# Optimization experiments

Measured on AMD Instinct MI355X. Metric: run time of the kernel, lower is better.

## Reference

```python
import jax, jax.numpy as jnp
import numpy as np

KERNEL_MUL = 2.0
KERNEL_NUM = 5
EPS = 1e-06


def setup_inputs() -> dict:
    key = jax.random.key(0)
    k1, k2 = jax.random.split(key)
    N, D = 4096, 256
    source = jax.random.normal(k1, (N, D), dtype=jnp.float32)
    target = jax.random.normal(k2, (N, D), dtype=jnp.float32)
    return {"source": source, "target": target}


def reference(source, target):
    n_src = source.shape[0]
    total = jnp.concatenate([source, target], axis=0)  # [2N, D]
    n = total.shape[0]
    # the broadcasted (total0 - total1)**2 sum, without the O(N^2*D) tensor).
    sq = jnp.sum(total * total, axis=1)  # [2N]
    L2 = sq[:, None] + sq[None, :] - 2.0 * (total @ total.T)  # [2N, 2N]
    # Bandwidth from detached distances (torch uses L2_distance.data).
    bandwidth = jax.lax.stop_gradient(jnp.sum(L2)) / (n * n - n)
    bandwidth = bandwidth / (KERNEL_MUL ** (KERNEL_NUM // 2))
    kernels = jnp.zeros_like(L2)
    for i in range(KERNEL_NUM):
        bw = bandwidth * (KERNEL_MUL ** i)
        kernels = kernels + jnp.exp(-L2 / (bw + EPS))
    XX = kernels[:n_src, :n_src]
    YY = kernels[n_src:, n_src:]
    XY = kernels[:n_src, n_src:]
    YX = kernels[n_src:, :n_src]
    return jnp.mean(XX + YY - XY - YX)
```

## Files before the change

### kernel.cpp

```cpp
#include <hip/hip_runtime.h>

#define N_TOT 8192
#define NS 4096
#define D 256
#define NB 64
#define NTRI (NB*(NB+1)/2)
#define HALF_B 32

typedef float f32x16 __attribute__((ext_vector_type(16)));
typedef float f32x2 __attribute__((ext_vector_type(2)));
typedef int i32x4 __attribute__((ext_vector_type(4)));
typedef int i32x8 __attribute__((ext_vector_type(8)));

__device__ __forceinline__ void gload16(const void* g, void* l) {
  __builtin_amdgcn_global_load_lds(
      (const __attribute__((address_space(1))) unsigned int*)g,
      (__attribute__((address_space(3))) unsigned int*)l,
      16, 0, 0);
}

__global__ void k_prep(const float* __restrict__ src, const float* __restrict__ tgt,
                       unsigned char* __restrict__ Xb, float* __restrict__ sqv,
                       float* __restrict__ pm, float* __restrict__ wsqp) {
  __shared__ float colacc[256];
  __shared__ float wred[4];
  int t = threadIdx.x, l = t & 63, w = t >> 6;
  colacc[t] = 0.f;
  __syncthreads();
  int base = blockIdx.x * 32;
  float c0 = 0.f, c1 = 0.f, c2 = 0.f, c3 = 0.f;
  float wsq = 0.f;
  #pragma unroll
  for (int r = 0; r < 8; ++r) {
    int row = base + w * 8 + r;
    const float* p = (row < NS) ? (src + (size_t)row * D) : (tgt + (size_t)(row - NS) * D);
    float4 v = ((const float4*)p)[l];
    int pk = __builtin_amdgcn_cvt_pk_fp8_f32(v.x, v.y, 0, false);
    pk = __builtin_amdgcn_cvt_pk_fp8_f32(v.z, v.w, pk, true);
    ((int*)(Xb + (size_t)row * D))[l] = pk;
    c0 += v.x; c1 += v.y; c2 += v.z; c3 += v.w;
    float s = fmaf(v.x, v.x, fmaf(v.y, v.y, fmaf(v.z, v.z, v.w * v.w)));
    for (int o = 32; o > 0; o >>= 1) s += __shfl_down(s, o, 64);
    if (l == 0) { sqv[row] = s; wsq += s; }
  }
  atomicAdd(&colacc[4 * l + 0], c0);
  atomicAdd(&colacc[4 * l + 1], c1);
  atomicAdd(&colacc[4 * l + 2], c2);
  atomicAdd(&colacc[4 * l + 3], c3);
  if (l == 0) wred[w] = wsq;
  __syncthreads();
  pm[blockIdx.x * 256 + t] = colacc[t];
  if (t == 0) wsqp[blockIdx.x] = (wred[0] + wred[1]) + (wred[2] + wred[3]);
}

__global__ void k_bw(const float* __restrict__ pm, const float* __restrict__ wsqp,
                     float* __restrict__ coef) {
  __shared__ double red[256];
  int t = threadIdx.x;
  float cs = 0.f;
  for (int b = 0; b < 256; ++b) cs += pm[b * 256 + t];
  red[t] = (double)cs * (double)cs;
  __syncthreads();
  for (int s = 128; s > 0; s >>= 1) {
    if (t < s) red[t] += red[t + s];
    __syncthreads();
  }
  double msq = red[0];
  __syncthreads();
  red[t] = (double)wsqp[t];
  __syncthreads();
  for (int s = 128; s > 0; s >>= 1) {
    if (t < s) red[t] += red[t + s];
    __syncthreads();
  }
  if (t == 0) {
    double Sv = red[0];
    double n = (double)N_TOT;
    double sumL2 = 2.0 * n * Sv - 2.0 * msq;
    double bw = sumL2 / (n * n - n) / 4.0;
    double c4 = 1.0 / (bw * 16.0 + 1e-6);
    coef[0] = (float)(c4 * 1.4426950408889634);
  }
}

__global__ __launch_bounds__(256) void k_main(
    const unsigned char* __restrict__ Xb, const float* __restrict__ sqv,
    const float* __restrict__ coef, float* __restrict__ bpart) {
  int b = blockIdx.x;
  int bi = (int)((2.f * NB + 1.f - sqrtf((float)((2 * NB + 1) * (2 * NB + 1) - 8 * b))) * 0.5f);
  if (bi < 0) bi = 0;
  if (bi > NB - 1) bi = NB - 1;
  while ((bi + 1) * (2 * NB - bi) / 2 <= b) ++bi;
  while (bi * (2 * NB - bi + 1) / 2 > b) --bi;
  int bj = bi + (b - bi * (2 * NB - bi + 1) / 2);

  __shared__ unsigned char ldsA[128 * 64];
  __shared__ unsigned char ldsB[128 * 64];
  __shared__ float sqA[128], sqB[128];
  __shared__ float redw[4];

  int t = threadIdx.x, l = t & 63, w = t >> 6;
  int lr = l & 31, half = l >> 5;
  int waveRow = w >> 1, waveCol = w & 1;

  if (t < 128) sqA[t] = sqv[bi * 128 + t];
  else         sqB[t - 128] = sqv[bj * 128 + (t - 128)];
  float A4 = coef[0];

  const unsigned char* arow = Xb + (size_t)bi * 128 * D;
  const unsigned char* brow = Xb + (size_t)bj * 128 * D;

  f32x16 acc[2][2] = {};
  int cLo = 2 * half, cHi = 2 * half + 1;

  for (int ko = 0; ko < 4; ++ko) {
    if (ko) __syncthreads();
    int kOff = ko * 64;
    #pragma unroll
    for (int p = 0; p < 2; ++p) {
      int seg = p * 256 + t;
      int row = seg >> 2;
      int kb = (seg & 3) ^ (row & 3) ^ ((row >> 2) & 3);
      int goff = row * D + kOff + kb * 16;
      gload16(arow + goff, &ldsA[(p * 256 + w * 64) * 16]);
      gload16(brow + goff, &ldsB[(p * 256 + w * 64) * 16]);
    }
    __syncthreads();
    i32x8 aF[2];
    #pragma unroll
    for (int rb = 0; rb < 2; ++rb) {
      int rowA = waveRow * 64 + rb * 32 + lr;
      int sw = (rowA & 3) ^ ((rowA >> 2) & 3);
      i32x4 lo = *(const i32x4*)&ldsA[rowA * 64 + (cLo ^ sw) * 16];
      i32x4 hi = *(const i32x4*)&ldsA[rowA * 64 + (cHi ^ sw) * 16];
      aF[rb] = (i32x8){lo.x, lo.y, lo.z, lo.w, hi.x, hi.y, hi.z, hi.w};
    }
    #pragma unroll
    for (int cb = 0; cb < 2; ++cb) {
      int rowB = waveCol * 64 + cb * 32 + lr;
      int sw = (rowB & 3) ^ ((rowB >> 2) & 3);
      i32x4 lo = *(const i32x4*)&ldsB[rowB * 64 + (cLo ^ sw) * 16];
      i32x4 hi = *(const i32x4*)&ldsB[rowB * 64 + (cHi ^ sw) * 16];
      i32x8 bF = (i32x8){lo.x, lo.y, lo.z, lo.w, hi.x, hi.y, hi.z, hi.w};
      #pragma unroll
      for (int rb = 0; rb < 2; ++rb)
        acc[rb][cb] = __builtin_amdgcn_mfma_scale_f32_32x32x64_f8f6f4(
            aF[rb], bF, acc[rb][cb], 0, 0, 0, 127, 0, 127);
    }
  }

  float c2A4 = 2.f * A4, nA4 = -A4;
  f32x2 lsum2 = {0.f, 0.f};
  bool diag = (bi == bj);
  #pragma unroll
  for (int cb = 0; cb < 2; ++cb) {
    int jj = waveCol * 64 + cb * 32 + lr;
    float bjv = nA4 * sqB[jj];
    #pragma unroll
    for (int rb = 0; rb < 2; ++rb) {
      #pragma unroll
      for (int r = 0; r < 16; r += 2) {
        int ii = waveRow * 64 + rb * 32 + (r & 3) + 8 * (r >> 2) + 4 * half;
        f32x2 dot2 = {acc[rb][cb][r], acc[rb][cb][r + 1]};
        f32x2 sq2 = {sqA[ii], sqA[ii + 1]};
        f32x2 tt = c2A4 * dot2 + (nA4 * sq2 + bjv);
        f32x2 e;
        e.x = __builtin_amdgcn_exp2f(tt.x);
        e.y = __builtin_amdgcn_exp2f(tt.y);
        f32x2 e2 = e * e, e4 = e2 * e2, e8 = e4 * e4, e16 = e8 * e8;
        f32x2 kern = ((e + e2) + (e4 + e8)) + e16;
        if (diag) {
          if (ii == jj) kern.x = 0.f;
          if (ii + 1 == jj) kern.y = 0.f;
        }
        lsum2 += kern;
      }
    }
  }
  float lsum = lsum2.x + lsum2.y;
  for (int o = 32; o > 0; o >>= 1) lsum += __shfl_down(lsum, o, 64);
  if (l == 0) redw[w] = lsum;
  __syncthreads();
  if (t == 0) {
    float tot = (redw[0] + redw[1]) + (redw[2] + redw[3]);
    float wgt = diag ? 1.f : 2.f;
    float sgn = ((bi < HALF_B) == (bj < HALF_B)) ? 1.f : -1.f;
    bpart[b] = tot * wgt * sgn;
  }
}

__global__ void k_final(const float* __restrict__ bpart, float* __restrict__ out) {
  __shared__ double red[256];
  int t = threadIdx.x;
  double s = 0.0;
  for (int k = 0; k < 9; ++k) {
    int idx = k * 256 + t;
    if (idx < NTRI) s += (double)bpart[idx];
  }
  red[t] = s;
  __syncthreads();
  for (int st = 128; st > 0; st >>= 1) {
    if (t < st) red[t] += red[t + st];
    __syncthreads();
  }
  if (t == 0) {
    double total = red[0] + 5.0 * (double)N_TOT;
    out[0] = (float)(total / ((double)NS * (double)NS));
  }
}

extern "C" void kernel_launch(void* const* d_in, const int* in_sizes, int n_in,
                              void* d_out, int out_size, void* d_ws, size_t ws_size,
                              hipStream_t stream) {
  const float* src = (const float*)d_in[0];
  const float* tgt = (const float*)d_in[1];
  float* out = (float*)d_out;
  char* ws = (char*)d_ws;
  unsigned char* Xb = (unsigned char*)ws;
  float* sqv  = (float*)(ws + (4u << 20));
  float* pm   = (float*)(ws + (4u << 20) + (32u << 10));
  float* wsqp = (float*)(ws + (4u << 20) + (288u << 10));
  float* coef = (float*)(ws + (4u << 20) + (289u << 10));
  float* bpart = (float*)(ws + (4u << 20) + (290u << 10));

  hipLaunchKernelGGL(k_prep, dim3(256), dim3(256), 0, stream, src, tgt, Xb, sqv, pm, wsqp);
  hipLaunchKernelGGL(k_bw, dim3(1), dim3(256), 0, stream, pm, wsqp, coef);
  hipLaunchKernelGGL(k_main, dim3(NTRI), dim3(256), 0, stream, Xb, sqv, coef, bpart);
  hipLaunchKernelGGL(k_final, dim3(1), dim3(256), 0, stream, bpart, out);
}
```

Baseline: 97.93 us.

## Fold bandwidth and final reductions into last-block tails via atomic counters

Removes the two single-block kernels (bandwidth computation and final sum) by having the last block to finish k_prep and k_main, detected with an atomic counter plus thread fences, perform those reductions. A memset resets the counters each call, so four kernel launches become one memset plus two kernels. It also adds a 4-blocks-per-SM occupancy hint to k_main's launch bounds and aligns its LDS buffers. The change trades launch gaps for an extra memset node, an atomic per block, and a serial tail reduction on the last block.

```diff
diff --git a/kernel.cpp b/kernel.cpp
--- a/kernel.cpp
+++ b/kernel.cpp
@@ -21,9 +21,12 @@
 
 __global__ void k_prep(const float* __restrict__ src, const float* __restrict__ tgt,
                        unsigned char* __restrict__ Xb, float* __restrict__ sqv,
-                       float* __restrict__ pm, float* __restrict__ wsqp) {
+                       float* __restrict__ pm, float* __restrict__ wsqp,
+                       float* __restrict__ coef, unsigned* __restrict__ cnt) {
   __shared__ float colacc[256];
   __shared__ float wred[4];
+  __shared__ double redD[256];
+  __shared__ unsigned isl;
   int t = threadIdx.x, l = t & 63, w = t >> 6;
   colacc[t] = 0.f;
   __syncthreads();
@@ -51,41 +54,47 @@
   __syncthreads();
   pm[blockIdx.x * 256 + t] = colacc[t];
   if (t == 0) wsqp[blockIdx.x] = (wred[0] + wred[1]) + (wred[2] + wred[3]);
-}
-
-__global__ void k_bw(const float* __restrict__ pm, const float* __restrict__ wsqp,
-                     float* __restrict__ coef) {
-  __shared__ double red[256];
-  int t = threadIdx.x;
-  float cs = 0.f;
-  for (int b = 0; b < 256; ++b) cs += pm[b * 256 + t];
-  red[t] = (double)cs * (double)cs;
-  __syncthreads();
-  for (int s = 128; s > 0; s >>= 1) {
-    if (t < s) red[t] += red[t + s];
-    __syncthreads();
-  }
-  double msq = red[0];
-  __syncthreads();
-  red[t] = (double)wsqp[t];
-  __syncthreads();
-  for (int s = 128; s > 0; s >>= 1) {
-    if (t < s) red[t] += red[t + s];
-    __syncthreads();
-  }
+
+  __syncthreads();
   if (t == 0) {
-    double Sv = red[0];
-    double n = (double)N_TOT;
-    double sumL2 = 2.0 * n * Sv - 2.0 * msq;
-    double bw = sumL2 / (n * n - n) / 4.0;
-    double c4 = 1.0 / (bw * 16.0 + 1e-6);
-    coef[0] = (float)(c4 * 1.4426950408889634);
-  }
-}
-
-__global__ __launch_bounds__(256) void k_main(
+    __threadfence();
+    isl = (atomicAdd(cnt, 1u) == 255u) ? 1u : 0u;
+  }
+  __syncthreads();
+  if (isl) {
+    if (t == 0) __threadfence();
+    __syncthreads();
+    float cs = 0.f;
+    for (int bb = 0; bb < 256; ++bb) cs += pm[bb * 256 + t];
+    redD[t] = (double)cs * (double)cs;
+    __syncthreads();
+    for (int s = 128; s > 0; s >>= 1) {
+      if (t < s) redD[t] += redD[t + s];
+      __syncthreads();
+    }
+    double msq = redD[0];
+    __syncthreads();
+    redD[t] = (double)wsqp[t];
+    __syncthreads();
+    for (int s = 128; s > 0; s >>= 1) {
+      if (t < s) redD[t] += redD[t + s];
+      __syncthreads();
+    }
+    if (t == 0) {
+      double Sv = redD[0];
+      double n = (double)N_TOT;
+      double sumL2 = 2.0 * n * Sv - 2.0 * msq;
+      double bw = sumL2 / (n * n - n) / 4.0;
+      double c4 = 1.0 / (bw * 16.0 + 1e-6);
+      coef[0] = (float)(c4 * 1.4426950408889634);
+    }
+  }
+}
+
+__global__ __launch_bounds__(256, 4) void k_main(
     const unsigned char* __restrict__ Xb, const float* __restrict__ sqv,
-    const float* __restrict__ coef, float* __restrict__ bpart) {
+    const float* __restrict__ coef, float* __restrict__ bpart,
+    unsigned* __restrict__ cnt, float* __restrict__ out) {
   int b = blockIdx.x;
   int bi = (int)((2.f * NB + 1.f - sqrtf((float)((2 * NB + 1) * (2 * NB + 1) - 8 * b))) * 0.5f);
   if (bi < 0) bi = 0;
@@ -94,10 +103,11 @@
   while (bi * (2 * NB - bi + 1) / 2 > b) --bi;
   int bj = bi + (b - bi * (2 * NB - bi + 1) / 2);
 
-  __shared__ unsigned char ldsA[128 * 64];
-  __shared__ unsigned char ldsB[128 * 64];
+  __shared__ __align__(16) unsigned char ldsA[128 * 64];
+  __shared__ __align__(16) unsigned char ldsB[128 * 64];
   __shared__ float sqA[128], sqB[128];
   __shared__ float redw[4];
+  __shared__ unsigned isl;
 
   int t = threadIdx.x, l = t & 63, w = t >> 6;
   int lr = l & 31, half = l >> 5;
@@ -187,25 +197,32 @@
     float sgn = ((bi < HALF_B) == (bj < HALF_B)) ? 1.f : -1.f;
     bpart[b] = tot * wgt * sgn;
   }
-}
-
-__global__ void k_final(const float* __restrict__ bpart, float* __restrict__ out) {
-  __shared__ double red[256];
-  int t = threadIdx.x;
-  double s = 0.0;
-  for (int k = 0; k < 9; ++k) {
-    int idx = k * 256 + t;
-    if (idx < NTRI) s += (double)bpart[idx];
-  }
-  red[t] = s;
-  __syncthreads();
-  for (int st = 128; st > 0; st >>= 1) {
-    if (t < st) red[t] += red[t + st];
-    __syncthreads();
-  }
+
+  __syncthreads();
   if (t == 0) {
-    double total = red[0] + 5.0 * (double)N_TOT;
-    out[0] = (float)(total / ((double)NS * (double)NS));
+    __threadfence();
+    isl = (atomicAdd(cnt, 1u) == (unsigned)(NTRI - 1)) ? 1u : 0u;
+  }
+  __syncthreads();
+  if (isl) {
+    if (t == 0) __threadfence();
+    __syncthreads();
+    double* redF = (double*)ldsA;
+    double s = 0.0;
+    for (int k = 0; k < 9; ++k) {
+      int idx = k * 256 + t;
+      if (idx < NTRI) s += (double)bpart[idx];
+    }
+    redF[t] = s;
+    __syncthreads();
+    for (int st = 128; st > 0; st >>= 1) {
+      if (t < st) redF[t] += redF[t + st];
+      __syncthreads();
+    }
+    if (t == 0) {
+      double total = redF[0] + 5.0 * (double)N_TOT;
+      out[0] = (float)(total / ((double)NS * (double)NS));
+    }
   }
 }
 
@@ -222,9 +239,9 @@
   float* wsqp = (float*)(ws + (4u << 20) + (288u << 10));
   float* coef = (float*)(ws + (4u << 20) + (289u << 10));
   float* bpart = (float*)(ws + (4u << 20) + (290u << 10));
-
-  hipLaunchKernelGGL(k_prep, dim3(256), dim3(256), 0, stream, src, tgt, Xb, sqv, pm, wsqp);
-  hipLaunchKernelGGL(k_bw, dim3(1), dim3(256), 0, stream, pm, wsqp, coef);
-  hipLaunchKernelGGL(k_main, dim3(NTRI), dim3(256), 0, stream, Xb, sqv, coef, bpart);
-  hipLaunchKernelGGL(k_final, dim3(1), dim3(256), 0, stream, bpart, out);
-}
+  unsigned* cnts = (unsigned*)(ws + (4u << 20) + (300u << 10));
+
+  hipMemsetAsync(cnts, 0, 8, stream);
+  hipLaunchKernelGGL(k_prep, dim3(256), dim3(256), 0, stream, src, tgt, Xb, sqv, pm, wsqp, coef, cnts);
+  hipLaunchKernelGGL(k_main, dim3(NTRI), dim3(256), 0, stream, Xb, sqv, coef, bpart, cnts + 1, out);
+}
```

New measurement: 135.5 us. 38.4% more time.

## Fuse bandwidth and final reductions into producer kernels via last-block atomics

Applied to the files above, without the earlier changes.

Removes the two single-block kernels (bandwidth computation and final sum) by having the last-arriving block of k_prep and k_main do the reduction. Partial sums are accumulated with double atomics and completion is detected with global counters that a memset clears first. k_prep also moves to 512 threads per block with 4 rows per wave. This cuts kernel launches and serial tail work, but adds a memset, atomic contention, and a dependence on memory-ordering correctness.

```diff
diff --git a/kernel.cpp b/kernel.cpp
--- a/kernel.cpp
+++ b/kernel.cpp
@@ -19,20 +19,24 @@
       16, 0, 0);
 }
 
-__global__ void k_prep(const float* __restrict__ src, const float* __restrict__ tgt,
-                       unsigned char* __restrict__ Xb, float* __restrict__ sqv,
-                       float* __restrict__ pm, float* __restrict__ wsqp) {
+__global__ __launch_bounds__(512) void k_prep(
+    const float* __restrict__ src, const float* __restrict__ tgt,
+    unsigned char* __restrict__ Xb, float* __restrict__ sqv,
+    double* __restrict__ colsum, double* __restrict__ wsqacc,
+    unsigned* __restrict__ cnt1, float* __restrict__ coef) {
   __shared__ float colacc[256];
-  __shared__ float wred[4];
+  __shared__ float wred[8];
+  __shared__ double red[256];
+  __shared__ int isl;
   int t = threadIdx.x, l = t & 63, w = t >> 6;
-  colacc[t] = 0.f;
+  if (t < 256) colacc[t] = 0.f;
   __syncthreads();
   int base = blockIdx.x * 32;
   float c0 = 0.f, c1 = 0.f, c2 = 0.f, c3 = 0.f;
   float wsq = 0.f;
   #pragma unroll
-  for (int r = 0; r < 8; ++r) {
-    int row = base + w * 8 + r;
+  for (int r = 0; r < 4; ++r) {
+    int row = base + w * 4 + r;
     const float* p = (row < NS) ? (src + (size_t)row * D) : (tgt + (size_t)(row - NS) * D);
     float4 v = ((const float4*)p)[l];
     int pk = __builtin_amdgcn_cvt_pk_fp8_f32(v.x, v.y, 0, false);
@@ -49,43 +53,42 @@
   atomicAdd(&colacc[4 * l + 3], c3);
   if (l == 0) wred[w] = wsq;
   __syncthreads();
-  pm[blockIdx.x * 256 + t] = colacc[t];
-  if (t == 0) wsqp[blockIdx.x] = (wred[0] + wred[1]) + (wred[2] + wred[3]);
-}
-
-__global__ void k_bw(const float* __restrict__ pm, const float* __restrict__ wsqp,
-                     float* __restrict__ coef) {
-  __shared__ double red[256];
-  int t = threadIdx.x;
-  float cs = 0.f;
-  for (int b = 0; b < 256; ++b) cs += pm[b * 256 + t];
-  red[t] = (double)cs * (double)cs;
-  __syncthreads();
-  for (int s = 128; s > 0; s >>= 1) {
-    if (t < s) red[t] += red[t + s];
+  if (t < 256) atomicAdd(&colsum[t], (double)colacc[t]);
+  if (t == 0) {
+    float ws8 = ((wred[0] + wred[1]) + (wred[2] + wred[3])) +
+                ((wred[4] + wred[5]) + (wred[6] + wred[7]));
+    atomicAdd(wsqacc, (double)ws8);
+  }
+  asm volatile("s_waitcnt vmcnt(0)" ::: "memory");
+  __syncthreads();
+  if (t == 0) isl = (atomicAdd(cnt1, 1u) == 255u) ? 1 : 0;
+  __syncthreads();
+  if (isl) {
+    if (t < 256) {
+      double d = atomicAdd(&colsum[t], 0.0);
+      red[t] = d * d;
+    }
     __syncthreads();
-  }
-  double msq = red[0];
-  __syncthreads();
-  red[t] = (double)wsqp[t];
-  __syncthreads();
-  for (int s = 128; s > 0; s >>= 1) {
-    if (t < s) red[t] += red[t + s];
-    __syncthreads();
-  }
-  if (t == 0) {
-    double Sv = red[0];
-    double n = (double)N_TOT;
-    double sumL2 = 2.0 * n * Sv - 2.0 * msq;
-    double bw = sumL2 / (n * n - n) / 4.0;
-    double c4 = 1.0 / (bw * 16.0 + 1e-6);
-    coef[0] = (float)(c4 * 1.4426950408889634);
+    for (int s = 128; s > 0; s >>= 1) {
+      if (t < s) red[t] += red[t + s];
+      __syncthreads();
+    }
+    if (t == 0) {
+      double msq = red[0];
+      double Sv = atomicAdd(wsqacc, 0.0);
+      double n = (double)N_TOT;
+      double sumL2 = 2.0 * n * Sv - 2.0 * msq;
+      double bw = sumL2 / (n * n - n) / 4.0;
+      double c4 = 1.0 / (bw * 16.0 + 1e-6);
+      coef[0] = (float)(c4 * 1.4426950408889634);
+    }
   }
 }
 
 __global__ __launch_bounds__(256) void k_main(
     const unsigned char* __restrict__ Xb, const float* __restrict__ sqv,
-    const float* __restrict__ coef, float* __restrict__ bpart) {
+    const float* __restrict__ coef, double* __restrict__ gbins,
+    unsigned* __restrict__ cnt2, float* __restrict__ out) {
   int b = blockIdx.x;
   int bi = (int)((2.f * NB + 1.f - sqrtf((float)((2 * NB + 1) * (2 * NB + 1) - 8 * b))) * 0.5f);
   if (bi < 0) bi = 0;
@@ -98,6 +101,7 @@
   __shared__ unsigned char ldsB[128 * 64];
   __shared__ float sqA[128], sqB[128];
   __shared__ float redw[4];
+  __shared__ int islast;
 
   int t = threadIdx.x, l = t & 63, w = t >> 6;
   int lr = l & 31, half = l >> 5;
@@ -185,27 +189,20 @@
     float tot = (redw[0] + redw[1]) + (redw[2] + redw[3]);
     float wgt = diag ? 1.f : 2.f;
     float sgn = ((bi < HALF_B) == (bj < HALF_B)) ? 1.f : -1.f;
-    bpart[b] = tot * wgt * sgn;
-  }
-}
-
-__global__ void k_final(const float* __restrict__ bpart, float* __restrict__ out) {
-  __shared__ double red[256];
-  int t = threadIdx.x;
-  double s = 0.0;
-  for (int k = 0; k < 9; ++k) {
-    int idx = k * 256 + t;
-    if (idx < NTRI) s += (double)bpart[idx];
-  }
-  red[t] = s;
-  __syncthreads();
-  for (int st = 128; st > 0; st >>= 1) {
-    if (t < st) red[t] += red[t + st];
-    __syncthreads();
-  }
-  if (t == 0) {
-    double total = red[0] + 5.0 * (double)N_TOT;
-    out[0] = (float)(total / ((double)NS * (double)NS));
+    atomicAdd(&gbins[b & 31], (double)(tot * wgt * sgn));
+    asm volatile("s_waitcnt vmcnt(0)" ::: "memory");
+    islast = (atomicAdd(cnt2, 1u) == (unsigned)(NTRI - 1)) ? 1 : 0;
+  }
+  __syncthreads();
+  if (islast) {
+    if (t < 32) {
+      double d = atomicAdd(&gbins[t], 0.0);
+      for (int o = 16; o > 0; o >>= 1) d += __shfl_down(d, o, 32);
+      if (t == 0) {
+        double total = d + 5.0 * (double)N_TOT;
+        out[0] = (float)(total / ((double)NS * (double)NS));
+      }
+    }
   }
 }
 
@@ -217,14 +214,18 @@
   float* out = (float*)d_out;
   char* ws = (char*)d_ws;
   unsigned char* Xb = (unsigned char*)ws;
-  float* sqv  = (float*)(ws + (4u << 20));
-  float* pm   = (float*)(ws + (4u << 20) + (32u << 10));
-  float* wsqp = (float*)(ws + (4u << 20) + (288u << 10));
-  float* coef = (float*)(ws + (4u << 20) + (289u << 10));
-  float* bpart = (float*)(ws + (4u << 20) + (290u << 10));
-
-  hipLaunchKernelGGL(k_prep, dim3(256), dim3(256), 0, stream, src, tgt, Xb, sqv, pm, wsqp);
-  hipLaunchKernelGGL(k_bw, dim3(1), dim3(256), 0, stream, pm, wsqp, coef);
-  hipLaunchKernelGGL(k_main, dim3(NTRI), dim3(256), 0, stream, Xb, sqv, coef, bpart);
-  hipLaunchKernelGGL(k_final, dim3(1), dim3(256), 0, stream, bpart, out);
-}
+  float* sqv = (float*)(ws + (4u << 20));
+  char* zr = ws + (4u << 20) + (64u << 10);
+  double* colsum  = (double*)zr;
+  double* wsqacc  = (double*)(zr + 2048);
+  double* gbins   = (double*)(zr + 2056);
+  unsigned* cnt1  = (unsigned*)(zr + 2312);
+  unsigned* cnt2  = (unsigned*)(zr + 2316);
+  float* coef     = (float*)(zr + 2320);
+
+  hipMemsetAsync(zr, 0, 2560, stream);
+  hipLaunchKernelGGL(k_prep, dim3(256), dim3(512), 0, stream,
+                     src, tgt, Xb, sqv, colsum, wsqacc, cnt1, coef);
+  hipLaunchKernelGGL(k_main, dim3(NTRI), dim3(256), 0, stream,
+                     Xb, sqv, coef, gbins, cnt2, out);
+}
```

Result: slower. 108.4 us (+10.7%).
